# Kernel tuning notes

Measured on AMD Instinct MI355X. Metric: run time of the kernel, lower is better.

Reference implementation:

```python
import jax, jax.numpy as jnp
import numpy as np

N_WIN = 232
T = 8
KERNEL = (2, 2, 2)
STRIDE = (2, 2, 2)
SLOPE = 25.0  # fast_sigmoid surrogate slope


@jax.custom_vjp
def spike(v):
    # heaviside(v) with fast-sigmoid surrogate gradient
    return (v > 0).astype(v.dtype)

def _spike_fwd(v):
    return spike(v), v

def _spike_bwd(v, g):
    return (g / (SLOPE * jnp.abs(v) + 1.0) ** 2,)

spike.defvjp(_spike_fwd, _spike_bwd)


def _avg_pool3d(x, kernel, stride):
    # x: (B, C, D, H, W), VALID pooling
    win = (1, 1) + tuple(kernel)
    st = (1, 1) + tuple(stride)
    s = jax.lax.reduce_window(x, 0.0, jax.lax.add, win, st, 'VALID')
    return s / float(np.prod(kernel))


def setup_inputs() -> dict:
    key = jax.random.key(0)
    ks = jax.random.split(key, 14)
    B, C, H, W = 64, 3, 32, 32
    input_dim, h0, h1, n_cls = 256, 256, 128, 6
    x = jax.random.normal(ks[0], (B, C, N_WIN, H, W), jnp.float32)
    W_in = jax.random.normal(ks[1], (h0, input_dim), jnp.float32) * 0.05
    b_in = jnp.zeros((h0,), jnp.float32)
    W_hid = jax.random.normal(ks[2], (h1, h0), jnp.float32) * 0.05
    b_hid = jnp.zeros((h1,), jnp.float32)
    in_feat = C * h1 * 14  # C * hidden[1] * D'
    W_out = jax.random.normal(ks[3], (n_cls, in_feat), jnp.float32) * 0.05
    b_out = jnp.zeros((n_cls,), jnp.float32)
    beta_in = jax.random.uniform(ks[4], (h0,), jnp.float32)
    thr_in = jax.random.uniform(ks[5], (h0,), jnp.float32)
    beta_hid = jax.random.uniform(ks[6], (h1,), jnp.float32)
    thr_hid = jax.random.uniform(ks[7], (h1,), jnp.float32)
    beta_out = jax.random.uniform(ks[8], (n_cls,), jnp.float32)
    return dict(x=x, W_in=W_in, b_in=b_in, W_hid=W_hid, b_hid=b_hid,
                W_out=W_out, b_out=b_out, beta_in=beta_in, thr_in=thr_in,
                beta_hid=beta_hid, thr_hid=thr_hid, beta_out=beta_out)


def _lif(mem, cur, beta, thr):
    # snntorch Leaky, reset-by-subtract; reset uses detached prev-mem spike
    reset = jax.lax.stop_gradient((mem > thr).astype(mem.dtype))
    mem = jnp.clip(beta, 0.0, 1.0) * mem + cur - reset * thr
    spk = spike(mem - thr)
    return spk, mem


def reference(x, W_in, b_in, W_hid, b_hid, W_out, b_out,
              beta_in, thr_in, beta_hid, thr_hid, beta_out):
    B, C, _, H, W = x.shape
    chunk = N_WIN // T  # 29
    # split depth into T chunks: (T, B, C, chunk, H, W)
    xt = x.reshape(B, C, T, chunk, H, W).transpose(2, 0, 1, 3, 4, 5)
    pooled = jax.vmap(lambda v: _avg_pool3d(v, KERNEL, STRIDE))(xt)  # (T,B,C,D',H',W')
    _, _, _, Dp, Hp, Wp = pooled.shape
    pr = pooled.reshape(T, B, C * Dp, Hp * Wp)
    # fc_in applied to all timesteps at once (recurrence-free)
    cur_in_all = jnp.einsum('tbnf,hf->tbnh', pr, W_in) + b_in  # (T,B,N,h0)

    h0 = W_in.shape[0]
    h1 = W_hid.shape[0]
    n_cls = W_out.shape[0]
    N = C * Dp
    mem_in0 = jnp.zeros((B, N, h0), x.dtype)
    mem_hid0 = jnp.zeros((B, N, h1), x.dtype)
    mem_out0 = jnp.zeros((B, n_cls), x.dtype)

    def step(carry, cur_in):
        mem_in, mem_hid, mem_out = carry
        spk_in, mem_in = _lif(mem_in, cur_in, beta_in, thr_in)
        cur_hid = jnp.einsum('bnh,gh->bng', spk_in, W_hid) + b_hid
        spk_hid, mem_hid = _lif(mem_hid, cur_hid, beta_hid, thr_hid)
        flat = spk_hid.reshape(spk_hid.shape[0], -1)  # (B, N*h1)
        cur_out = flat @ W_out.T + b_out
        spk_out, mem_out = _lif(mem_out, cur_out, beta_out, jnp.float32(1.0))
        return (mem_in, mem_hid, mem_out), spk_out

    _, spk_rec = jax.lax.scan(step, (mem_in0, mem_hid0, mem_out0), cur_in_all)
    return spk_rec  # (T, B, n_classes)
```

## Files before the change

### kernel.cpp

```cpp
#include <hip/hip_runtime.h>

#define T_STEPS 8
#define NROW    42
#define BN      2688
#define H0      256
#define H1      128
#define NCLS    6
#define KFLAT   5376


#define SW(r)   ((r) + ((r) >> 5) * 4)
#define LDR     140

__global__ __launch_bounds__(256) void pool_kernel(const float* __restrict__ x,
                                                   float* __restrict__ pr) {
    int idx = blockIdx.x * 256 + threadIdx.x;
    int f   = idx & 255;
    int wp  = f & 15, hp = f >> 4;
    int rest = idx >> 8;
    int dp = rest % 14;
    int r2 = rest / 14;
    int c  = r2 % 3;
    int r3 = r2 / 3;
    int b  = r3 & 63;
    int t  = r3 >> 6;
    const float* base = x + ((long)b * 712704 + (long)c * 237568
                          + (long)(t * 29 + 2 * dp) * 1024
                          + (2 * hp) * 32 + 2 * wp);
    float2 v0 = *(const float2*)(base);
    float2 v1 = *(const float2*)(base + 32);
    float2 v2 = *(const float2*)(base + 1024);
    float2 v3 = *(const float2*)(base + 1056);
    float s = v0.x + v0.y + v1.x + v1.y + v2.x + v2.y + v3.x + v3.y;
    int m = (b * NROW + c * 14 + dp) * 8 + t;
    pr[(long)m * 256 + f] = s * 0.125f;
}

__global__ __launch_bounds__(256, 2) void gemm_lif(const float* __restrict__ A,
                                                   const float* __restrict__ B,
                                                   const float* __restrict__ bias,
                                                   const float* __restrict__ beta,
                                                   const float* __restrict__ thr,
                                                   float* __restrict__ spk,
                                                   int N, int K) {
    __shared__ float At[16 * LDR];
    __shared__ float Bt[16 * LDR];
    int tid = threadIdx.x;
    int m0 = blockIdx.y * 128, n0 = blockIdx.x * 128;

    int sr = tid >> 1, sq = tid & 1;
    int scol = SW(sr);
    const float* Ap = A + (long)(m0 + sr) * K + sq * 8;
    const float* Bp = B + (long)(n0 + sr) * K + sq * 8;

    int tm = tid & 15, tn = tid >> 4;
    int ca = SW(tm * 8);
    int cb = SW(tn * 8);

    float acc[8][8] = {};

    for (int k0 = 0; k0 < K; k0 += 16) {
        float4 a0 = *(const float4*)(Ap + k0);
        float4 a1 = *(const float4*)(Ap + k0 + 4);
        float4 b0 = *(const float4*)(Bp + k0);
        float4 b1 = *(const float4*)(Bp + k0 + 4);
        __syncthreads();
        int kb = sq * 8;
        At[(kb + 0) * LDR + scol] = a0.x; At[(kb + 1) * LDR + scol] = a0.y;
        At[(kb + 2) * LDR + scol] = a0.z; At[(kb + 3) * LDR + scol] = a0.w;
        At[(kb + 4) * LDR + scol] = a1.x; At[(kb + 5) * LDR + scol] = a1.y;
        At[(kb + 6) * LDR + scol] = a1.z; At[(kb + 7) * LDR + scol] = a1.w;
        Bt[(kb + 0) * LDR + scol] = b0.x; Bt[(kb + 1) * LDR + scol] = b0.y;
        Bt[(kb + 2) * LDR + scol] = b0.z; Bt[(kb + 3) * LDR + scol] = b0.w;
        Bt[(kb + 4) * LDR + scol] = b1.x; Bt[(kb + 5) * LDR + scol] = b1.y;
        Bt[(kb + 6) * LDR + scol] = b1.z; Bt[(kb + 7) * LDR + scol] = b1.w;
        __syncthreads();
#pragma unroll
        for (int k = 0; k < 16; ++k) {
            float4 av0 = *(const float4*)&At[k * LDR + ca];
            float4 av1 = *(const float4*)&At[k * LDR + ca + 4];
            float4 bv0 = *(const float4*)&Bt[k * LDR + cb];
            float4 bv1 = *(const float4*)&Bt[k * LDR + cb + 4];
            float am[8] = {av0.x, av0.y, av0.z, av0.w, av1.x, av1.y, av1.z, av1.w};
            float bn_[8] = {bv0.x, bv0.y, bv0.z, bv0.w, bv1.x, bv1.y, bv1.z, bv1.w};
#pragma unroll
            for (int i = 0; i < 8; ++i)
#pragma unroll
                for (int j = 0; j < 8; ++j)
                    acc[i][j] = fmaf(am[i], bn_[j], acc[i][j]);
        }
    }

#pragma unroll
    for (int c = 0; c < 8; ++c) {
        int h = n0 + tn * 8 + c;
        float be = fminf(fmaxf(beta[h], 0.f), 1.f);
        float th = thr[h];
        float bi = bias[h];
        float mem = 0.f;
#pragma unroll
        for (int t = 0; t < T_STEPS; ++t) {
            float cur = acc[t][c] + bi;
            float reset = (mem > th) ? th : 0.f;
            mem = be * mem + cur - reset;
            acc[t][c] = ((mem - th) > 0.f) ? 1.f : 0.f;
        }
    }
    int rbase = m0 + tm * 8;
#pragma unroll
    for (int t = 0; t < T_STEPS; ++t) {
        long row = rbase + t;
        int col = n0 + tn * 8;
        float4 o0 = {acc[t][0], acc[t][1], acc[t][2], acc[t][3]};
        float4 o1 = {acc[t][4], acc[t][5], acc[t][6], acc[t][7]};
        *(float4*)&spk[row * N + col]     = o0;
        *(float4*)&spk[row * N + col + 4] = o1;
    }
}

__global__ __launch_bounds__(256) void out_gemm(const float* __restrict__ spkh,
                                                const float* __restrict__ W_out,
                                                const float* __restrict__ b_out,
                                                float* __restrict__ cur_out) {
    __shared__ float part[256][8];
    int row = blockIdx.x;
    int t = row >> 6, b = row & 63;
    int tid = threadIdx.x;
    float acc[6] = {0.f, 0.f, 0.f, 0.f, 0.f, 0.f};
    for (int j = tid; j < KFLAT; j += 256) {
        int n = j >> 7, h = j & 127;
        float s = spkh[((long)(b * NROW + n) * 8 + t) * 128 + h];
#pragma unroll
        for (int c = 0; c < 6; ++c)
            acc[c] = fmaf(s, W_out[c * KFLAT + j], acc[c]);
    }
#pragma unroll
    for (int c = 0; c < 6; ++c) part[tid][c] = acc[c];
    __syncthreads();
    for (int off = 128; off > 0; off >>= 1) {
        if (tid < off) {
#pragma unroll
            for (int c = 0; c < 6; ++c) part[tid][c] += part[tid + off][c];
        }
        __syncthreads();
    }
    if (tid < 6) cur_out[row * 6 + tid] = part[0][tid] + b_out[tid];
}

__global__ void lif_out_kernel(const float* __restrict__ cur_out,
                               const float* __restrict__ beta_out,
                               float* __restrict__ out) {
    int j = threadIdx.x;
    if (j >= 384) return;
    int cls = j % 6;
    float be = fminf(fmaxf(beta_out[cls], 0.f), 1.f);
    float mem = 0.f;
#pragma unroll
    for (int t = 0; t < T_STEPS; ++t) {
        float cur = cur_out[t * 384 + j];
        float reset = (mem > 1.f) ? 1.f : 0.f;
        mem = be * mem + cur - reset;
        out[t * 384 + j] = ((mem - 1.f) > 0.f) ? 1.f : 0.f;
    }
}

extern "C" void kernel_launch(void* const* d_in, const int* in_sizes, int n_in,
                              void* d_out, int out_size, void* d_ws, size_t ws_size,
                              hipStream_t stream) {
    (void)in_sizes; (void)n_in; (void)out_size; (void)ws_size;
    const float* x        = (const float*)d_in[0];
    const float* W_in     = (const float*)d_in[1];
    const float* b_in     = (const float*)d_in[2];
    const float* W_hid    = (const float*)d_in[3];
    const float* b_hid    = (const float*)d_in[4];
    const float* W_out    = (const float*)d_in[5];
    const float* b_out    = (const float*)d_in[6];
    const float* beta_in  = (const float*)d_in[7];
    const float* thr_in   = (const float*)d_in[8];
    const float* beta_hid = (const float*)d_in[9];
    const float* thr_hid  = (const float*)d_in[10];
    const float* beta_out = (const float*)d_in[11];
    float* out = (float*)d_out;

    float* buf0 = (float*)d_ws;
    float* buf1 = buf0 + 5505024;
    float* curo = buf1 + 5505024;

    pool_kernel<<<21504, 256, 0, stream>>>(x, buf0);
    gemm_lif<<<dim3(2, 168), 256, 0, stream>>>(buf0, W_in, b_in, beta_in, thr_in,
                                               buf1, 256, 256);
    gemm_lif<<<dim3(1, 168), 256, 0, stream>>>(buf1, W_hid, b_hid, beta_hid, thr_hid,
                                               buf0, 128, 256);
    out_gemm<<<512, 256, 0, stream>>>(buf0, W_out, b_out, curo);
    lif_out_kernel<<<1, 384, 0, stream>>>(curo, beta_out, out);
}
```

Baseline: 388.0 us.

## Fuse avg-pool into first GEMM+LIF and shrink GEMM tiles to 64 rows

The pooling pass now happens inside the first GEMM+LIF kernel: each thread sums 2x2x2 input windows and writes the pooled values straight into the shared A tile. This removes the pooled intermediate's global write and read-back. The first kernel uses 512-thread blocks covering 64 rows by all 256 hidden units, and the second GEMM moves to 64-row tiles with 4x8 per-thread outputs to launch more blocks. The trade-off is smaller per-thread register tiles, so arithmetic intensity drops and strided pooled loads sit in the GEMM's main loop.

```diff
diff --git a/kernel.cpp b/kernel.cpp
--- a/kernel.cpp
+++ b/kernel.cpp
@@ -5,116 +5,195 @@
 #define BN      2688
 #define H0      256
 #define H1      128
-#define NCLS    6
 #define KFLAT   5376
 
 
-#define SW(r)   ((r) + ((r) >> 5) * 4)
-#define LDR     140
-
-__global__ __launch_bounds__(256) void pool_kernel(const float* __restrict__ x,
-                                                   float* __restrict__ pr) {
-    int idx = blockIdx.x * 256 + threadIdx.x;
-    int f   = idx & 255;
-    int wp  = f & 15, hp = f >> 4;
-    int rest = idx >> 8;
-    int dp = rest % 14;
-    int r2 = rest / 14;
-    int c  = r2 % 3;
-    int r3 = r2 / 3;
-    int b  = r3 & 63;
-    int t  = r3 >> 6;
-    const float* base = x + ((long)b * 712704 + (long)c * 237568
-                          + (long)(t * 29 + 2 * dp) * 1024
-                          + (2 * hp) * 32 + 2 * wp);
-    float2 v0 = *(const float2*)(base);
-    float2 v1 = *(const float2*)(base + 32);
-    float2 v2 = *(const float2*)(base + 1024);
-    float2 v3 = *(const float2*)(base + 1056);
-    float s = v0.x + v0.y + v1.x + v1.y + v2.x + v2.y + v3.x + v3.y;
-    int m = (b * NROW + c * 14 + dp) * 8 + t;
-    pr[(long)m * 256 + f] = s * 0.125f;
-}
-
-__global__ __launch_bounds__(256, 2) void gemm_lif(const float* __restrict__ A,
-                                                   const float* __restrict__ B,
-                                                   const float* __restrict__ bias,
-                                                   const float* __restrict__ beta,
-                                                   const float* __restrict__ thr,
-                                                   float* __restrict__ spk,
-                                                   int N, int K) {
-    __shared__ float At[16 * LDR];
-    __shared__ float Bt[16 * LDR];
+#define SWA(r)  ((r) + ((r) >> 5) * 4)
+
+__global__ __launch_bounds__(512, 4) void pool_gemm_lif(
+        const float* __restrict__ x,
+        const float* __restrict__ B,
+        const float* __restrict__ bias,
+        const float* __restrict__ beta,
+        const float* __restrict__ thr,
+        float* __restrict__ spk) {
+    __shared__ float At[16 * 68];
+    __shared__ float Bt[16 * 284];
     int tid = threadIdx.x;
-    int m0 = blockIdx.y * 128, n0 = blockIdx.x * 128;
-
-    int sr = tid >> 1, sq = tid & 1;
-    int scol = SW(sr);
-    const float* Ap = A + (long)(m0 + sr) * K + sq * 8;
-    const float* Bp = B + (long)(n0 + sr) * K + sq * 8;
-
-    int tm = tid & 15, tn = tid >> 4;
-    int ca = SW(tm * 8);
-    int cb = SW(tn * 8);
-
-    float acc[8][8] = {};
-
-    for (int k0 = 0; k0 < K; k0 += 16) {
-        float4 a0 = *(const float4*)(Ap + k0);
-        float4 a1 = *(const float4*)(Ap + k0 + 4);
-        float4 b0 = *(const float4*)(Bp + k0);
-        float4 b1 = *(const float4*)(Bp + k0 + 4);
-        __syncthreads();
-        int kb = sq * 8;
-        At[(kb + 0) * LDR + scol] = a0.x; At[(kb + 1) * LDR + scol] = a0.y;
-        At[(kb + 2) * LDR + scol] = a0.z; At[(kb + 3) * LDR + scol] = a0.w;
-        At[(kb + 4) * LDR + scol] = a1.x; At[(kb + 5) * LDR + scol] = a1.y;
-        At[(kb + 6) * LDR + scol] = a1.z; At[(kb + 7) * LDR + scol] = a1.w;
-        Bt[(kb + 0) * LDR + scol] = b0.x; Bt[(kb + 1) * LDR + scol] = b0.y;
-        Bt[(kb + 2) * LDR + scol] = b0.z; Bt[(kb + 3) * LDR + scol] = b0.w;
-        Bt[(kb + 4) * LDR + scol] = b1.x; Bt[(kb + 5) * LDR + scol] = b1.y;
-        Bt[(kb + 6) * LDR + scol] = b1.z; Bt[(kb + 7) * LDR + scol] = b1.w;
+    int gbase = blockIdx.x * 8;
+
+    int wp = tid & 15;
+    int q  = tid >> 4;
+    const float* xb0;
+    const float* xb1;
+    int mloc0 = q * 2, mloc1 = q * 2 + 1;
+    {
+        int g = gbase + (mloc0 >> 3);
+        int t = mloc0 & 7;
+        int b = g / 42, r = g - b * 42;
+        int c = r / 14, dp = r - c * 14;
+        xb0 = x + ((long)b * 712704 + (long)c * 237568
+                + (long)(t * 29 + 2 * dp) * 1024 + 2 * wp);
+    }
+    {
+        int g = gbase + (mloc1 >> 3);
+        int t = mloc1 & 7;
+        int b = g / 42, r = g - b * 42;
+        int c = r / 14, dp = r - c * 14;
+        xb1 = x + ((long)b * 712704 + (long)c * 237568
+                + (long)(t * 29 + 2 * dp) * 1024 + 2 * wp);
+    }
+    int acol0 = SWA(mloc0), acol1 = SWA(mloc1);
+
+    int bn0 = tid >> 1;
+    int bq  = tid & 1;
+    const float* Bp = B + (long)bn0 * 256 + bq * 8;
+    int bcol = SWA(bn0);
+
+    int tm = tid & 7, tn = tid >> 3;
+    int ca = SWA(tm * 8);
+    int cb = SWA(tn * 4);
+
+    float acc[8][4] = {};
+
+    for (int k0 = 0; k0 < 256; k0 += 16) {
+        int hp = k0 >> 4;
+        const float* p0 = xb0 + hp * 64;
+        const float* p1 = xb1 + hp * 64;
+        float2 a00 = *(const float2*)(p0);
+        float2 a01 = *(const float2*)(p0 + 32);
+        float2 a02 = *(const float2*)(p0 + 1024);
+        float2 a03 = *(const float2*)(p0 + 1056);
+        float2 a10 = *(const float2*)(p1);
+        float2 a11 = *(const float2*)(p1 + 32);
+        float2 a12 = *(const float2*)(p1 + 1024);
+        float2 a13 = *(const float2*)(p1 + 1056);
+        float4 w0 = *(const float4*)(Bp + k0);
+        float4 w1 = *(const float4*)(Bp + k0 + 4);
+        __syncthreads();
+        float s0 = a00.x + a00.y + a01.x + a01.y + a02.x + a02.y + a03.x + a03.y;
+        float s1 = a10.x + a10.y + a11.x + a11.y + a12.x + a12.y + a13.x + a13.y;
+        At[wp * 68 + acol0] = s0 * 0.125f;
+        At[wp * 68 + acol1] = s1 * 0.125f;
+        int kb = bq * 8;
+        Bt[(kb + 0) * 284 + bcol] = w0.x; Bt[(kb + 1) * 284 + bcol] = w0.y;
+        Bt[(kb + 2) * 284 + bcol] = w0.z; Bt[(kb + 3) * 284 + bcol] = w0.w;
+        Bt[(kb + 4) * 284 + bcol] = w1.x; Bt[(kb + 5) * 284 + bcol] = w1.y;
+        Bt[(kb + 6) * 284 + bcol] = w1.z; Bt[(kb + 7) * 284 + bcol] = w1.w;
         __syncthreads();
 #pragma unroll
         for (int k = 0; k < 16; ++k) {
-            float4 av0 = *(const float4*)&At[k * LDR + ca];
-            float4 av1 = *(const float4*)&At[k * LDR + ca + 4];
-            float4 bv0 = *(const float4*)&Bt[k * LDR + cb];
-            float4 bv1 = *(const float4*)&Bt[k * LDR + cb + 4];
+            float4 av0 = *(const float4*)&At[k * 68 + ca];
+            float4 av1 = *(const float4*)&At[k * 68 + ca + 4];
+            float4 bv  = *(const float4*)&Bt[k * 284 + cb];
             float am[8] = {av0.x, av0.y, av0.z, av0.w, av1.x, av1.y, av1.z, av1.w};
-            float bn_[8] = {bv0.x, bv0.y, bv0.z, bv0.w, bv1.x, bv1.y, bv1.z, bv1.w};
+            float bb[4] = {bv.x, bv.y, bv.z, bv.w};
 #pragma unroll
             for (int i = 0; i < 8; ++i)
 #pragma unroll
-                for (int j = 0; j < 8; ++j)
-                    acc[i][j] = fmaf(am[i], bn_[j], acc[i][j]);
-        }
-    }
-
-#pragma unroll
-    for (int c = 0; c < 8; ++c) {
-        int h = n0 + tn * 8 + c;
+                for (int j = 0; j < 4; ++j)
+                    acc[i][j] = fmaf(am[i], bb[j], acc[i][j]);
+        }
+    }
+
+#pragma unroll
+    for (int j = 0; j < 4; ++j) {
+        int h = tn * 4 + j;
         float be = fminf(fmaxf(beta[h], 0.f), 1.f);
         float th = thr[h];
         float bi = bias[h];
         float mem = 0.f;
 #pragma unroll
         for (int t = 0; t < T_STEPS; ++t) {
-            float cur = acc[t][c] + bi;
+            float cur = acc[t][j] + bi;
             float reset = (mem > th) ? th : 0.f;
             mem = be * mem + cur - reset;
-            acc[t][c] = ((mem - th) > 0.f) ? 1.f : 0.f;
+            acc[t][j] = ((mem - th) > 0.f) ? 1.f : 0.f;
+        }
+    }
+    int rbase = blockIdx.x * 64 + tm * 8;
+#pragma unroll
+    for (int t = 0; t < T_STEPS; ++t) {
+        float4 o = {acc[t][0], acc[t][1], acc[t][2], acc[t][3]};
+        *(float4*)&spk[(long)(rbase + t) * 256 + tn * 4] = o;
+    }
+}
+
+__global__ __launch_bounds__(256, 4) void gemm_lif64(
+        const float* __restrict__ A,
+        const float* __restrict__ B,
+        const float* __restrict__ bias,
+        const float* __restrict__ beta,
+        const float* __restrict__ thr,
+        float* __restrict__ spk) {
+    __shared__ float At[16 * 68];
+    __shared__ float Bt[16 * 140];
+    int tid = threadIdx.x;
+    int m0 = blockIdx.x * 64;
+
+    int sr = tid >> 2, sq = tid & 3;
+    const float* Ap = A + (long)(m0 + sr) * 256 + sq * 4;
+    int acolS = SWA(sr);
+
+    int br = tid >> 1, bq = tid & 1;
+    const float* Bp = B + (long)br * 256 + bq * 8;
+    int bcolS = SWA(br);
+
+    int tm = tid & 7, tn = tid >> 3;
+    int ca = SWA(tm * 8);
+    int cb = SWA(tn * 4);
+
+    float acc[8][4] = {};
+
+    for (int k0 = 0; k0 < 256; k0 += 16) {
+        float4 a  = *(const float4*)(Ap + k0);
+        float4 w0 = *(const float4*)(Bp + k0);
+        float4 w1 = *(const float4*)(Bp + k0 + 4);
+        __syncthreads();
+        int ka = sq * 4;
+        At[(ka + 0) * 68 + acolS] = a.x; At[(ka + 1) * 68 + acolS] = a.y;
+        At[(ka + 2) * 68 + acolS] = a.z; At[(ka + 3) * 68 + acolS] = a.w;
+        int kb = bq * 8;
+        Bt[(kb + 0) * 140 + bcolS] = w0.x; Bt[(kb + 1) * 140 + bcolS] = w0.y;
+        Bt[(kb + 2) * 140 + bcolS] = w0.z; Bt[(kb + 3) * 140 + bcolS] = w0.w;
+        Bt[(kb + 4) * 140 + bcolS] = w1.x; Bt[(kb + 5) * 140 + bcolS] = w1.y;
+        Bt[(kb + 6) * 140 + bcolS] = w1.z; Bt[(kb + 7) * 140 + bcolS] = w1.w;
+        __syncthreads();
+#pragma unroll
+        for (int k = 0; k < 16; ++k) {
+            float4 av0 = *(const float4*)&At[k * 68 + ca];
+            float4 av1 = *(const float4*)&At[k * 68 + ca + 4];
+            float4 bv  = *(const float4*)&Bt[k * 140 + cb];
+            float am[8] = {av0.x, av0.y, av0.z, av0.w, av1.x, av1.y, av1.z, av1.w};
+            float bb[4] = {bv.x, bv.y, bv.z, bv.w};
+#pragma unroll
+            for (int i = 0; i < 8; ++i)
+#pragma unroll
+                for (int j = 0; j < 4; ++j)
+                    acc[i][j] = fmaf(am[i], bb[j], acc[i][j]);
+        }
+    }
+
+#pragma unroll
+    for (int j = 0; j < 4; ++j) {
+        int h = tn * 4 + j;
+        float be = fminf(fmaxf(beta[h], 0.f), 1.f);
+        float th = thr[h];
+        float bi = bias[h];
+        float mem = 0.f;
+#pragma unroll
+        for (int t = 0; t < T_STEPS; ++t) {
+            float cur = acc[t][j] + bi;
+            float reset = (mem > th) ? th : 0.f;
+            mem = be * mem + cur - reset;
+            acc[t][j] = ((mem - th) > 0.f) ? 1.f : 0.f;
         }
     }
     int rbase = m0 + tm * 8;
 #pragma unroll
     for (int t = 0; t < T_STEPS; ++t) {
-        long row = rbase + t;
-        int col = n0 + tn * 8;
-        float4 o0 = {acc[t][0], acc[t][1], acc[t][2], acc[t][3]};
-        float4 o1 = {acc[t][4], acc[t][5], acc[t][6], acc[t][7]};
-        *(float4*)&spk[row * N + col]     = o0;
-        *(float4*)&spk[row * N + col + 4] = o1;
+        float4 o = {acc[t][0], acc[t][1], acc[t][2], acc[t][3]};
+        *(float4*)&spk[(long)(rbase + t) * 128 + tn * 4] = o;
     }
 }
 
@@ -186,11 +265,8 @@
     float* buf1 = buf0 + 5505024;
     float* curo = buf1 + 5505024;
 
-    pool_kernel<<<21504, 256, 0, stream>>>(x, buf0);
-    gemm_lif<<<dim3(2, 168), 256, 0, stream>>>(buf0, W_in, b_in, beta_in, thr_in,
-                                               buf1, 256, 256);
-    gemm_lif<<<dim3(1, 168), 256, 0, stream>>>(buf1, W_hid, b_hid, beta_hid, thr_hid,
-                                               buf0, 128, 256);
+    pool_gemm_lif<<<336, 512, 0, stream>>>(x, W_in, b_in, beta_in, thr_in, buf1);
+    gemm_lif64<<<336, 256, 0, stream>>>(buf1, W_hid, b_hid, beta_hid, thr_hid, buf0);
     out_gemm<<<512, 256, 0, stream>>>(buf0, W_out, b_out, curo);
     lif_out_kernel<<<1, 384, 0, stream>>>(curo, beta_out, out);
 }
```

Measured after the change: 355.8 us. -8.3%, faster.
